# Optimization experiments

Hardware: AMD Instinct MI355X
Metric: run time of the kernel (lower is better)

Reference implementation:

```python
import jax, jax.numpy as jnp
from jax import lax
import numpy as np

DN = ('NCHW', 'OIHW', 'NCHW')

def conv(x, w, b, stride, pad):
    y = lax.conv_general_dilated(x, w, (stride, stride), [(pad, pad), (pad, pad)], dimension_numbers=DN)
    return y if b is None else y + b[None, :, None, None]

def conv_transpose(x, w, b):
    # torch ConvTranspose2d(k=4, s=2, p=1); w in torch layout (Cin, Cout, 4, 4)
    w_f = jnp.flip(w, (2, 3)).transpose(1, 0, 2, 3)  # -> OIHW, flipped
    y = lax.conv_general_dilated(x, w_f, (1, 1), [(2, 2), (2, 2)], lhs_dilation=(2, 2), dimension_numbers=DN)
    return y + b[None, :, None, None]

def res_stack(x, w3, w1, n_layers=2):
    # shared weights across layers (ModuleList([layer]*n) aliases one module)
    for _ in range(n_layers):
        h = conv(jax.nn.relu(x), w3, None, 1, 1)
        h = conv(jax.nn.relu(h), w1, None, 1, 0)
        x = x + h
    return jax.nn.relu(x)

def setup_inputs() -> dict:
    key = jax.random.key(0)
    ks = jax.random.split(key, 16)
    s = 0.02
    d = {
        'x': jax.random.normal(ks[0], (32, 3, 256, 256), jnp.float32),
        'enc_w1': jax.random.normal(ks[1], (128, 3, 4, 4), jnp.float32) * s,
        'enc_b1': jnp.zeros((128,), jnp.float32),
        'enc_w2': jax.random.normal(ks[2], (256, 128, 4, 4), jnp.float32) * s,
        'enc_b2': jnp.zeros((256,), jnp.float32),
        'enc_w3': jax.random.normal(ks[3], (512, 256, 4, 4), jnp.float32) * s,
        'enc_b3': jnp.zeros((512,), jnp.float32),
        'enc_res_w3': jax.random.normal(ks[4], (32, 512, 3, 3), jnp.float32) * s,
        'enc_res_w1': jax.random.normal(ks[5], (512, 32, 1, 1), jnp.float32) * s,
        'prevq_w': jax.random.normal(ks[6], (64, 512, 1, 1), jnp.float32) * s,
        'prevq_b': jnp.zeros((64,), jnp.float32),
        'emb': jax.random.normal(ks[7], (512, 64), jnp.float32),
        'dec_w1': jax.random.normal(ks[8], (64, 256, 4, 4), jnp.float32) * s,
        'dec_b1': jnp.zeros((256,), jnp.float32),
        'dec_res_w3': jax.random.normal(ks[9], (32, 256, 3, 3), jnp.float32) * s,
        'dec_res_w1': jax.random.normal(ks[10], (256, 32, 1, 1), jnp.float32) * s,
        'dec_w2': jax.random.normal(ks[11], (256, 128, 4, 4), jnp.float32) * s,
        'dec_b2': jnp.zeros((128,), jnp.float32),
        'dec_w3': jax.random.normal(ks[12], (128, 3, 4, 4), jnp.float32) * s,
        'dec_b3': jnp.zeros((3,), jnp.float32),
    }
    return d

def vqvae_fwd(x, enc_w1, enc_b1, enc_w2, enc_b2, enc_w3, enc_b3, enc_res_w3, enc_res_w1,
              prevq_w, prevq_b, emb, dec_w1, dec_b1, dec_res_w3, dec_res_w1,
              dec_w2, dec_b2, dec_w3, dec_b3):
    # encoder
    z = jax.nn.relu(conv(x, enc_w1, enc_b1, 2, 1))
    z = jax.nn.relu(conv(z, enc_w2, enc_b2, 2, 1))
    z = conv(z, enc_w3, enc_b3, 2, 1)
    z = res_stack(z, enc_res_w3, enc_res_w1)
    z_e = conv(z, prevq_w, prevq_b, 1, 0)  # (B, D=64, 32, 32)
    # vector quantiser
    B, C, H, W = z_e.shape
    x_flat = z_e.reshape(B, C, H * W).transpose(0, 2, 1)  # (B, HW, D)
    d2 = (jnp.sum(x_flat ** 2, -1, keepdims=True)
          - 2.0 * jnp.einsum('bnd,kd->bnk', x_flat, emb)
          + jnp.sum(emb ** 2, -1))
    idx = jnp.argmin(d2, axis=2)  # (B, HW)
    z_q_flat = emb[idx]  # (B, HW, D)
    z_q = z_q_flat.transpose(0, 2, 1).reshape(B, C, H, W)
    sg = lax.stop_gradient
    q_loss = jnp.mean((sg(z_q_flat) - x_flat) ** 2) + jnp.mean((z_q_flat - sg(x_flat)) ** 2)
    # decoder
    y = conv_transpose(z_q, dec_w1, dec_b1)  # (B, 256, 64, 64)
    y = res_stack(y, dec_res_w3, dec_res_w1)
    y = jax.nn.relu(conv_transpose(y, dec_w2, dec_b2))
    y = conv_transpose(y, dec_w3, dec_b3)  # (B, 3, 256, 256)
    return y, q_loss

def reference(x, enc_w1, enc_b1, enc_w2, enc_b2, enc_w3, enc_b3, enc_res_w3, enc_res_w1,
              prevq_w, prevq_b, emb, dec_w1, dec_b1, dec_res_w3, dec_res_w1,
              dec_w2, dec_b2, dec_w3, dec_b3):
    return vqvae_fwd(x, enc_w1, enc_b1, enc_w2, enc_b2, enc_w3, enc_b3, enc_res_w3, enc_res_w1,
                     prevq_w, prevq_b, emb, dec_w1, dec_b1, dec_res_w3, dec_res_w1,
                     dec_w2, dec_b2, dec_w3, dec_b3)
```

## Files before the change

kernel.cpp:

```cpp
#include <hip/hip_runtime.h>

typedef __attribute__((ext_vector_type(8))) short short8;
typedef __attribute__((ext_vector_type(4))) float f32x4;
typedef __attribute__((ext_vector_type(4))) unsigned int uint4v;

__device__ __forceinline__ unsigned short f2bf(float f) {
  unsigned u = __builtin_bit_cast(unsigned, f);
  u = (u + 0x7FFFu + ((u >> 16) & 1u)) >> 16;
  return (unsigned short)u;
}
__device__ __forceinline__ float bf2f(unsigned short h) {
  unsigned u = ((unsigned)h) << 16;
  return __builtin_bit_cast(float, u);
}

template<int TMT, int MODE, bool SPLIT, bool RELU_IN, bool RELU_OUT, bool BIAS, bool ACCUM>
__global__ __launch_bounds__(256) void k_mfconv(
    const float* __restrict__ in, const unsigned short* __restrict__ wp,
    const float* __restrict__ bias, float* __restrict__ out,
    int Ci, int inW, int inH, int pWSH, int pHWSH,
    int Co, int ntap, int ntt,
    unsigned syp, unsigned sxp,
    int outW, int outHW) {
  const int tid  = threadIdx.x;
  const int lane = tid & 63, wave = tid >> 6;
  const int pW  = 1 << pWSH;
  const int pHW = 1 << pHWSH;
  const int inHW = inW * inH;
  const int nk32 = Ci >> 5;
  const int KS   = (nk32 >= 2) ? 2 : 1;
  const int NITS = 4 * KS;
  const int cpt  = nk32 / KS;
  const int total = ntap * cpt;

  int bx = blockIdx.x;
  const int gx = gridDim.x;
  if ((gx & 7) == 0) bx = (bx & 7) * (gx >> 3) + (bx >> 3);
  const int n0  = bx * 64;
  const int coG = blockIdx.y;
  const int ph  = (MODE == 1) ? blockIdx.z : 0;
  const int tap0 = (MODE == 1) ? ph * 4 : 0;
  const int pdy = ph >> 1, pdx = ph & 1;

  constexpr int NPL = SPLIT ? 2 : 1;
  constexpr int PL = 64 * 70;
  __shared__ __align__(16) unsigned short Bs[2 * NPL * PL];

  const int px  = lane;
  const int p   = n0 + px;
  const int img = p >> pHWSH;
  const int rem = p & (pHW - 1);
  const int y   = rem >> pWSH;
  const int x   = rem & (pW - 1);
  const size_t base_img = (size_t)img * Ci * inHW;

  constexpr int NTO = (TMT == 4) ? 4 : 2;
  const int mt = (TMT == 4) ? wave : (wave & 1);
  const int ntb = (TMT == 4) ? 0 : ((wave >> 1) * 2);
  f32x4 acc[NTO];
#pragma unroll
  for (int u = 0; u < NTO; ++u) acc[u] = (f32x4){0.f, 0.f, 0.f, 0.f};

  const int cp = wave;
  float v[16];

  auto ldr = [&](int tap_, int chunk_) {
    const int T = tap0 + tap_;
    const int dy = (int)((syp >> (2 * T)) & 3u) - 1;
    const int dx = (int)((sxp >> (2 * T)) & 3u) - 1;
    const int ys = (MODE == 2) ? (2 * y + dy) : (y + dy);
    const int xs = (MODE == 2) ? (2 * x + dx) : (x + dx);
    const bool ok = ((unsigned)ys < (unsigned)inH) && ((unsigned)xs < (unsigned)inW);
    const float* __restrict__ ipb = in + base_img + (ptrdiff_t)ys * inW + xs;
    const int ci0 = chunk_ * (KS * 32);
#pragma unroll
    for (int it2 = 0; it2 < 8; ++it2) {
      if (it2 >= NITS) break;
      const int cl = 2 * (cp + 4 * it2);
      float a = 0.f, b = 0.f;
      if (ok) {
        a = ipb[(size_t)(ci0 + cl) * inHW];
        b = ipb[(size_t)(ci0 + cl + 1) * inHW];
      }
      if (RELU_IN) { a = fmaxf(a, 0.f); b = fmaxf(b, 0.f); }
      v[2 * it2] = a; v[2 * it2 + 1] = b;
    }
  };
  auto pwr = [&](int b) {
#pragma unroll
    for (int it2 = 0; it2 < 8; ++it2) {
      if (it2 >= NITS) break;
      const int cl = 2 * (cp + 4 * it2);
      float a = v[2 * it2], c = v[2 * it2 + 1];
      unsigned short h0 = f2bf(a), h1 = f2bf(c);
      *(unsigned*)&Bs[(b * NPL) * PL + px * 70 + cl] = (unsigned)h0 | ((unsigned)h1 << 16);
      if (SPLIT) {
        unsigned short l0 = f2bf(a - bf2f(h0)), l1 = f2bf(c - bf2f(h1));
        *(unsigned*)&Bs[(b * NPL + 1) * PL + px * 70 + cl] = (unsigned)l0 | ((unsigned)l1 << 16);
      }
    }
  };

  ldr(0, 0);
  pwr(0);
  __syncthreads();

  int tap = 0, chunk = 0;
  for (int it = 0; it < total; ++it) {
    const int b = it & 1;
    const int T = tap0 + tap;
    short8 ah[2], al[2];
#pragma unroll
    for (int s = 0; s < 2; ++s) {
      if (s >= KS) break;
      const int cic = chunk * KS + s;
      size_t abase;
      if (SPLIT) abase = ((((size_t)coG * ntt + T) * nk32 + cic) * 2 * TMT + mt) * 512;
      else       abase = ((((size_t)coG * ntt + T) * nk32 + cic) * TMT + mt) * 512;
      ah[s] = *(const short8*)(wp + abase + (size_t)lane * 8);
      if (SPLIT) al[s] = *(const short8*)(wp + abase + (size_t)TMT * 512 + (size_t)lane * 8);
    }
    int tap2 = tap, chunk2 = chunk + 1;
    if (chunk2 == cpt) { chunk2 = 0; tap2 = tap + 1; }
    const bool more = (it + 1 < total);
    if (more) ldr(tap2, chunk2);
#pragma unroll
    for (int s = 0; s < 2; ++s) {
      if (s >= KS) break;
#pragma unroll
      for (int u = 0; u < NTO; ++u) {
        const int row = 16 * (ntb + u) + (lane & 15);
        const unsigned* bp = (const unsigned*)&Bs[(b * NPL) * PL + row * 70 + s * 32 + (lane >> 4) * 8];
        uint4v hv = {bp[0], bp[1], bp[2], bp[3]};
        short8 bh = __builtin_bit_cast(short8, hv);
        acc[u] = __builtin_amdgcn_mfma_f32_16x16x32_bf16(ah[s], bh, acc[u], 0, 0, 0);
        if (SPLIT) {
          const unsigned* bpl = bp + (PL >> 1);
          uint4v lv = {bpl[0], bpl[1], bpl[2], bpl[3]};
          short8 bl = __builtin_bit_cast(short8, lv);
          acc[u] = __builtin_amdgcn_mfma_f32_16x16x32_bf16(al[s], bh, acc[u], 0, 0, 0);
          acc[u] = __builtin_amdgcn_mfma_f32_16x16x32_bf16(ah[s], bl, acc[u], 0, 0, 0);
        }
      }
    }
    if (more) {
      pwr(b ^ 1);
      __syncthreads();
    }
    tap = tap2; chunk = chunk2;
  }

#pragma unroll
  for (int u = 0; u < NTO; ++u) {
    const int nt = ntb + u;
    const int pn = n0 + nt * 16 + (lane & 15);
    const int img2 = pn >> pHWSH;
    const int rem2 = pn & (pHW - 1);
    const int y2 = rem2 >> pWSH, x2 = rem2 & (pW - 1);
    int oy, ox;
    if (MODE == 1) { oy = 2 * y2 + pdy; ox = 2 * x2 + pdx; }
    else           { oy = y2;           ox = x2; }
#pragma unroll
    for (int r = 0; r < 4; ++r) {
      const int co = coG * (TMT * 16) + mt * 16 + (lane >> 4) * 4 + r;
      float val = acc[u][r];
      if (BIAS) val += bias[co];
      if (RELU_OUT) val = fmaxf(val, 0.f);
      size_t oi = ((size_t)img2 * Co + co) * outHW + (size_t)oy * outW + ox;
      if (ACCUM) out[oi] += val; else out[oi] = val;
    }
  }
}

template<bool SPLIT>
__global__ __launch_bounds__(256) void k_pack_o(
    const float* __restrict__ w, unsigned short* __restrict__ p,
    int Co, int Ci, int ntap, int TMT, int E) {
  int i = blockIdx.x * 256 + threadIdx.x;
  if (i >= E) return;
  const int NC = Ci >> 5;
  int j = i & 7, lane = (i >> 3) & 63, r = i >> 9;
  int mt = r % TMT; r /= TMT;
  int sp = 0;
  if (SPLIT) { sp = r % 2; r /= 2; }
  int cic = r % NC; r /= NC;
  int T = r % ntap; int coG = r / ntap;
  int co = coG * (TMT * 16) + mt * 16 + (lane & 15);
  int ci = cic * 32 + (lane >> 4) * 8 + j;
  float wv = w[((size_t)co * Ci + ci) * ntap + T];
  unsigned short hv = f2bf(wv);
  p[i] = (SPLIT && sp == 1) ? f2bf(wv - bf2f(hv)) : hv;
}

__global__ __launch_bounds__(256) void k_pack_ct(
    const float* __restrict__ w, unsigned short* __restrict__ p,
    int Ci, int Co, int TMT, int E) {
  int i = blockIdx.x * 256 + threadIdx.x;
  if (i >= E) return;
  const int NC = Ci >> 5;
  int j = i & 7, lane = (i >> 3) & 63, r = i >> 9;
  int mt = r % TMT; r /= TMT;
  int cic = r % NC; r /= NC;
  int T = r % 16;   int coG = r / 16;
  int phx = T >> 2, t = T & 3;
  int dy = phx >> 1, dx = phx & 1, ty = t >> 1, tx = t & 1;
  int ky = 2 * ty + 1 - dy, kx = 2 * tx + 1 - dx;
  int co = coG * (TMT * 16) + mt * 16 + (lane & 15);
  int ci = cic * 32 + (lane >> 4) * 8 + j;
  p[i] = f2bf(w[(((size_t)ci * Co + co) * 4 + ky) * 4 + kx]);
}

template<int COB, bool RELU_OUT>
__global__ __launch_bounds__(256) void k_conv4(
    const float* __restrict__ in, const float* __restrict__ w,
    const float* __restrict__ bias, float* __restrict__ out,
    int N, int Ci, int Hi, int Wi, int Co) {
  const int Ho = Hi >> 1, Wo = Wi >> 1;
  const int ow = blockIdx.x * 16 + (threadIdx.x & 15);
  const int oh = blockIdx.y * 16 + (threadIdx.x >> 4);
  const int zcnt = Co / COB;
  const int co0 = (blockIdx.z % zcnt) * COB;
  const int n   = blockIdx.z / zcnt;
  if (oh >= Ho || ow >= Wo) return;
  const float* __restrict__ ip = in + (size_t)n * Ci * Hi * Wi;
  float acc[COB];
#pragma unroll
  for (int j = 0; j < COB; ++j) acc[j] = bias[co0 + j];
  const int ih0 = 2 * oh - 1, iw0 = 2 * ow - 1;
  for (int ci = 0; ci < Ci; ++ci) {
    const float* __restrict__ ic = ip + (size_t)ci * Hi * Wi;
    float v[16];
#pragma unroll
    for (int kh = 0; kh < 4; ++kh) {
      const int ih = ih0 + kh;
      const bool hok = (unsigned)ih < (unsigned)Hi;
      const float* __restrict__ irow = ic + (long)ih * Wi;
#pragma unroll
      for (int kw = 0; kw < 4; ++kw) {
        const int iw = iw0 + kw;
        v[kh * 4 + kw] = (hok && (unsigned)iw < (unsigned)Wi) ? irow[iw] : 0.f;
      }
    }
#pragma unroll
    for (int j = 0; j < COB; ++j) {
      const float* __restrict__ wc = w + ((size_t)(co0 + j) * Ci + ci) * 16;
#pragma unroll
      for (int t = 0; t < 16; ++t) acc[j] = fmaf(v[t], wc[t], acc[j]);
    }
  }
#pragma unroll
  for (int j = 0; j < COB; ++j) {
    float a = acc[j];
    if (RELU_OUT) a = fmaxf(a, 0.f);
    out[(((size_t)n * Co + co0 + j) * Ho + oh) * Wo + ow] = a;
  }
}

template<int COB, bool RELU_IN, int CSPLIT>
__global__ __launch_bounds__(256) void k_conv3(
    const float* __restrict__ in, const float* __restrict__ w,
    float* __restrict__ out, int N, int Ci, int H, int W, int Co) {
  const int ow = blockIdx.x * 16 + (threadIdx.x & 15);
  const int oh = blockIdx.y * 16 + (threadIdx.x >> 4);
  const int zcnt = Co / COB;
  const int z = blockIdx.z;
  const int cs  = z % CSPLIT;
  const int co0 = ((z / CSPLIT) % zcnt) * COB;
  const int n   = z / (CSPLIT * zcnt);
  if (oh >= H || ow >= W) return;
  const int CPS = Ci / CSPLIT;
  const float* __restrict__ ip = in + (size_t)n * Ci * H * W;
  float acc[COB];
#pragma unroll
  for (int j = 0; j < COB; ++j) acc[j] = 0.f;
  for (int ci = cs * CPS; ci < (cs + 1) * CPS; ++ci) {
    const float* __restrict__ ic = ip + (size_t)ci * H * W;
    float v[9];
#pragma unroll
    for (int kh = 0; kh < 3; ++kh) {
      const int ih = oh - 1 + kh;
      const bool hok = (unsigned)ih < (unsigned)H;
      const float* __restrict__ irow = ic + (long)ih * W;
#pragma unroll
      for (int kw = 0; kw < 3; ++kw) {
        const int iw = ow - 1 + kw;
        float t = (hok && (unsigned)iw < (unsigned)W) ? irow[iw] : 0.f;
        if (RELU_IN) t = fmaxf(t, 0.f);
        v[kh * 3 + kw] = t;
      }
    }
#pragma unroll
    for (int j = 0; j < COB; ++j) {
      const float* __restrict__ wc = w + ((size_t)(co0 + j) * Ci + ci) * 9;
#pragma unroll
      for (int t = 0; t < 9; ++t) acc[j] = fmaf(v[t], wc[t], acc[j]);
    }
  }
#pragma unroll
  for (int j = 0; j < COB; ++j) {
    size_t oi = (((size_t)n * Co + co0 + j) * H + oh) * W + ow;
    if (CSPLIT > 1) atomicAdd(&out[oi], acc[j]);
    else out[oi] = acc[j];
  }
}

template<int COB, bool RELU_IN, bool ACCUM>
__global__ __launch_bounds__(256) void k_conv1(
    const float* __restrict__ in, const float* __restrict__ w,
    const float* __restrict__ bias, float* __restrict__ out,
    int N, int Ci, int P, int Co) {
  const int p = blockIdx.x * 256 + threadIdx.x;
  const int co0 = blockIdx.y * COB;
  const int n = blockIdx.z;
  if (p >= P) return;
  float acc[COB];
#pragma unroll
  for (int j = 0; j < COB; ++j) acc[j] = bias ? bias[co0 + j] : 0.f;
  const float* __restrict__ ip = in + (size_t)n * Ci * P + p;
#pragma unroll 8
  for (int ci = 0; ci < Ci; ++ci) {
    float v = ip[(size_t)ci * P];
    if (RELU_IN) v = fmaxf(v, 0.f);
#pragma unroll
    for (int j = 0; j < COB; ++j)
      acc[j] = fmaf(v, w[(size_t)(co0 + j) * Ci + ci], acc[j]);
  }
#pragma unroll
  for (int j = 0; j < COB; ++j) {
    size_t oi = ((size_t)n * Co + co0 + j) * P + p;
    if (ACCUM) out[oi] += acc[j]; else out[oi] = acc[j];
  }
}

template<int COB, bool RELU_IN, bool RELU_OUT>
__global__ __launch_bounds__(256) void k_convT(
    const float* __restrict__ in, const float* __restrict__ w,
    const float* __restrict__ bias, float* __restrict__ out,
    int N, int Ci, int Hi, int Wi, int Co) {
  const int Ho = Hi * 2, Wo = Wi * 2;
  const int x = blockIdx.x * 16 + (threadIdx.x & 15);
  const int y = blockIdx.y * 16 + (threadIdx.x >> 4);
  const int zcnt = Co / COB;
  const int co0 = (blockIdx.z % zcnt) * COB;
  const int n   = blockIdx.z / zcnt;
  if (x >= Wi || y >= Hi) return;
  const float* __restrict__ ip = in + (size_t)n * Ci * Hi * Wi;
  float a00[COB], a01[COB], a10[COB], a11[COB];
#pragma unroll
  for (int j = 0; j < COB; ++j) {
    float b = bias[co0 + j];
    a00[j] = b; a01[j] = b; a10[j] = b; a11[j] = b;
  }
  const bool r0 = y > 0, r2 = y + 1 < Hi, c0 = x > 0, c2 = x + 1 < Wi;
#pragma unroll 2
  for (int ci = 0; ci < Ci; ++ci) {
    const float* __restrict__ ic = ip + (size_t)ci * Hi * Wi + (size_t)y * Wi + x;
    float v00 = 0.f, v01 = 0.f, v02 = 0.f, v10 = 0.f, v12 = 0.f,
          v20 = 0.f, v21 = 0.f, v22 = 0.f;
    float v11 = ic[0];
    if (c0) v10 = ic[-1];
    if (c2) v12 = ic[1];
    if (r0) { v01 = ic[-Wi]; if (c0) v00 = ic[-Wi - 1]; if (c2) v02 = ic[-Wi + 1]; }
    if (r2) { v21 = ic[Wi];  if (c0) v20 = ic[Wi - 1];  if (c2) v22 = ic[Wi + 1]; }
    if (RELU_IN) {
      v00 = fmaxf(v00, 0.f); v01 = fmaxf(v01, 0.f); v02 = fmaxf(v02, 0.f);
      v10 = fmaxf(v10, 0.f); v11 = fmaxf(v11, 0.f); v12 = fmaxf(v12, 0.f);
      v20 = fmaxf(v20, 0.f); v21 = fmaxf(v21, 0.f); v22 = fmaxf(v22, 0.f);
    }
#pragma unroll
    for (int j = 0; j < COB; ++j) {
      const float* __restrict__ wc = w + ((size_t)ci * Co + co0 + j) * 16;
      a00[j] = fmaf(v11, wc[5],  fmaf(v10, wc[7],  fmaf(v01, wc[13], fmaf(v00, wc[15], a00[j]))));
      a01[j] = fmaf(v12, wc[4],  fmaf(v11, wc[6],  fmaf(v02, wc[12], fmaf(v01, wc[14], a01[j]))));
      a10[j] = fmaf(v21, wc[1],  fmaf(v20, wc[3],  fmaf(v11, wc[9],  fmaf(v10, wc[11], a10[j]))));
      a11[j] = fmaf(v22, wc[0],  fmaf(v21, wc[2],  fmaf(v12, wc[8],  fmaf(v11, wc[10], a11[j]))));
    }
  }
#pragma unroll
  for (int j = 0; j < COB; ++j) {
    size_t b = ((size_t)n * Co + co0 + j) * Ho;
    float o00 = a00[j], o01 = a01[j], o10 = a10[j], o11 = a11[j];
    if (RELU_OUT) {
      o00 = fmaxf(o00, 0.f); o01 = fmaxf(o01, 0.f);
      o10 = fmaxf(o10, 0.f); o11 = fmaxf(o11, 0.f);
    }
    out[(b + 2 * y) * Wo + 2 * x]         = o00;
    out[(b + 2 * y) * Wo + 2 * x + 1]     = o01;
    out[(b + 2 * y + 1) * Wo + 2 * x]     = o10;
    out[(b + 2 * y + 1) * Wo + 2 * x + 1] = o11;
  }
}

__global__ __launch_bounds__(256, 2) void k_vq(
    const float* __restrict__ ze, const float* __restrict__ emb,
    float* __restrict__ zq, float* __restrict__ loss) {
  __shared__ float e2s[512];
  const int tid = threadIdx.x;
  for (int k = tid; k < 512; k += 256) {
    const f32x4* e4 = (const f32x4*)(emb + (size_t)k * 64);
    float s = 0.f;
#pragma unroll
    for (int dq = 0; dq < 16; ++dq) {
      f32x4 ev = e4[dq];
      s = fmaf(ev[0], ev[0], s); s = fmaf(ev[1], ev[1], s);
      s = fmaf(ev[2], ev[2], s); s = fmaf(ev[3], ev[3], s);
    }
    e2s[k] = s;
  }
  __syncthreads();
  const int p = blockIdx.x * 256 + tid;
  const int n = p >> 10, px = p & 1023;
  float xv[64];
  const float* __restrict__ zp = ze + (size_t)n * 64 * 1024 + px;
#pragma unroll
  for (int d = 0; d < 64; ++d) xv[d] = zp[(size_t)d * 1024];
  float best = 1e30f; int bi = 0;
  for (int k = 0; k < 512; ++k) {
    const f32x4* e4 = (const f32x4*)(emb + (size_t)k * 64);
    float dot = 0.f;
#pragma unroll
    for (int dq = 0; dq < 16; ++dq) {
      f32x4 ev = e4[dq];
      dot = fmaf(xv[4 * dq],     ev[0], dot);
      dot = fmaf(xv[4 * dq + 1], ev[1], dot);
      dot = fmaf(xv[4 * dq + 2], ev[2], dot);
      dot = fmaf(xv[4 * dq + 3], ev[3], dot);
    }
    float sc = fmaf(-2.f, dot, e2s[k]);
    if (sc < best) { best = sc; bi = k; }
  }
  const float* __restrict__ eb = emb + (size_t)bi * 64;
  float* __restrict__ qp = zq + (size_t)n * 64 * 1024 + px;
  float l = 0.f;
#pragma unroll
  for (int d = 0; d < 64; ++d) {
    float ev = eb[d];
    qp[(size_t)d * 1024] = ev;
    float df = ev - xv[d];
    l = fmaf(df, df, l);
  }
#pragma unroll
  for (int off = 32; off > 0; off >>= 1) l += __shfl_down(l, off, 64);
  if ((tid & 63) == 0) atomicAdd(loss, l * (2.f / 2097152.f));
}

__global__ __launch_bounds__(64) void k_vq64(
    const float* __restrict__ ze, const float* __restrict__ emb,
    float* __restrict__ zq, float* __restrict__ loss,
    int N, int P, int K) {
  const int t = blockIdx.x * 64 + threadIdx.x;
  if (t >= N * P) return;
  const int n = t / P, p = t % P;
  float xv[64];
  const float* __restrict__ zp = ze + (size_t)n * 64 * P + p;
#pragma unroll
  for (int d = 0; d < 64; ++d) xv[d] = zp[(size_t)d * P];
  float best = 1e30f; int bi = 0;
  for (int k = 0; k < K; ++k) {
    const float* __restrict__ e = emb + (size_t)k * 64;
    float dot = 0.f, e2 = 0.f;
#pragma unroll
    for (int d = 0; d < 64; ++d) {
      float ev = e[d];
      dot = fmaf(xv[d], ev, dot);
      e2  = fmaf(ev, ev, e2);
    }
    float score = e2 - 2.f * dot;
    if (score < best) { best = score; bi = k; }
  }
  const float* __restrict__ eb = emb + (size_t)bi * 64;
  float* __restrict__ qp = zq + (size_t)n * 64 * P + p;
  float l = 0.f;
#pragma unroll
  for (int d = 0; d < 64; ++d) {
    float ev = eb[d];
    qp[(size_t)d * P] = ev;
    float df = ev - xv[d];
    l = fmaf(df, df, l);
  }
#pragma unroll
  for (int off = 32; off > 0; off >>= 1) l += __shfl_down(l, off, 64);
  if ((threadIdx.x & 63) == 0) atomicAdd(loss, l * (2.f / 2097152.f));
}

extern "C" void kernel_launch(void* const* d_in, const int* in_sizes, int n_in,
                              void* d_out, int out_size, void* d_ws, size_t ws_size,
                              hipStream_t stream) {
  const float* x    = (const float*)d_in[0];
  const float* ew1  = (const float*)d_in[1];
  const float* eb1  = (const float*)d_in[2];
  const float* ew2  = (const float*)d_in[3];
  const float* eb2  = (const float*)d_in[4];
  const float* ew3  = (const float*)d_in[5];
  const float* eb3  = (const float*)d_in[6];
  const float* erw3 = (const float*)d_in[7];
  const float* erw1 = (const float*)d_in[8];
  const float* pqw  = (const float*)d_in[9];
  const float* pqb  = (const float*)d_in[10];
  const float* emb  = (const float*)d_in[11];
  const float* dw1  = (const float*)d_in[12];
  const float* db1  = (const float*)d_in[13];
  const float* drw3 = (const float*)d_in[14];
  const float* drw1 = (const float*)d_in[15];
  const float* dw2  = (const float*)d_in[16];
  const float* db2  = (const float*)d_in[17];
  const float* dw3  = (const float*)d_in[18];
  const float* db3  = (const float*)d_in[19];
  float* out = (float*)d_out;
  char*  ws  = (char*)d_ws;
  float* loss = out + 6291456;
  const size_t MiB = 1048576ull, KiB = 1024ull;

  dim3 blk(256);
  hipMemsetAsync(loss, 0, 4, stream);

  unsigned syct = 0, sxct = 0;
  for (int T = 0; T < 16; ++T) {
    int phx = T >> 2, dy = phx >> 1, dx = phx & 1, t = T & 3, ty = t >> 1, tx = t & 1;
    int sy = (dy == 0) ? (ty ? -1 : 0) : (ty ? 0 : 1);
    int sx = (dx == 0) ? (tx ? -1 : 0) : (tx ? 0 : 1);
    syct |= (unsigned)(sy + 1) << (2 * T);
    sxct |= (unsigned)(sx + 1) << (2 * T);
  }
  unsigned syc3 = 0, sxc3 = 0;
  for (int t = 0; t < 9; ++t) {
    syc3 |= (unsigned)(t / 3) << (2 * t);
    sxc3 |= (unsigned)(t % 3) << (2 * t);
  }
  unsigned syc4 = 0, sxc4 = 0;
  for (int t = 0; t < 16; ++t) {
    syc4 |= (unsigned)(t / 4) << (2 * t);
    sxc4 |= (unsigned)(t % 4) << (2 * t);
  }
  const unsigned sy1 = 1, sx1 = 1;

  auto packs = [&](char* PB) {
    unsigned short* e2p   = (unsigned short*)(PB);
    unsigned short* e3p   = (unsigned short*)(PB + 2048 * KiB);
    unsigned short* erc3p = (unsigned short*)(PB + 10240 * KiB);
    unsigned short* erc1p = (unsigned short*)(PB + 10816 * KiB);
    unsigned short* pqp   = (unsigned short*)(PB + 10880 * KiB);
    unsigned short* d1p   = (unsigned short*)(PB + 11008 * KiB);
    unsigned short* d2p   = (unsigned short*)(PB + 11520 * KiB);
    unsigned short* dc3p  = (unsigned short*)(PB + 12544 * KiB);
    unsigned short* dc1p  = (unsigned short*)(PB + 12688 * KiB);
    k_pack_o<true ><<<dim3(1048576 / 256), blk, 0, stream>>>(ew2,  e2p,  256, 128, 16, 4, 1048576);
    k_pack_o<true ><<<dim3(4194304 / 256), blk, 0, stream>>>(ew3,  e3p,  512, 256, 16, 4, 4194304);
    k_pack_o<true ><<<dim3(294912 / 256),  blk, 0, stream>>>(erw3, erc3p, 32, 512,  9, 2, 294912);
    k_pack_o<true ><<<dim3(32768 / 256),   blk, 0, stream>>>(erw1, erc1p, 512, 32,  1, 4, 32768);
    k_pack_o<true ><<<dim3(65536 / 256),   blk, 0, stream>>>(pqw,  pqp,   64, 512,  1, 4, 65536);
    k_pack_ct<<<dim3(262144 / 256), blk, 0, stream>>>(dw1, d1p, 64, 256, 4, 262144);
    k_pack_ct<<<dim3(524288 / 256), blk, 0, stream>>>(dw2, d2p, 256, 128, 4, 524288);
    k_pack_o<false><<<dim3(73728 / 256),   blk, 0, stream>>>(drw3, dc3p,  32, 256,  9, 2, 73728);
    k_pack_o<false><<<dim3(8192 / 256),    blk, 0, stream>>>(drw1, dc1p, 256, 32,  1, 4, 8192);
  };

  if (ws_size >= 498ull * MiB) {
    float* z1 = (float*)ws;
    float* z2 = (float*)(ws + 256 * MiB);
    float* z3 = (float*)(ws + 384 * MiB);
    float* h  = (float*)(ws + 448 * MiB);
    float* ze = (float*)(ws + 452 * MiB);
    float* zq = (float*)(ws + 460 * MiB);
    float* hd = (float*)(ws + 468 * MiB);
    char*  PB = ws + 484 * MiB;
    unsigned short* e2p   = (unsigned short*)(PB);
    unsigned short* e3p   = (unsigned short*)(PB + 2048 * KiB);
    unsigned short* erc3p = (unsigned short*)(PB + 10240 * KiB);
    unsigned short* erc1p = (unsigned short*)(PB + 10816 * KiB);
    unsigned short* pqp   = (unsigned short*)(PB + 10880 * KiB);
    unsigned short* d1p   = (unsigned short*)(PB + 11008 * KiB);
    unsigned short* d2p   = (unsigned short*)(PB + 11520 * KiB);
    unsigned short* dc3p  = (unsigned short*)(PB + 12544 * KiB);
    unsigned short* dc1p  = (unsigned short*)(PB + 12688 * KiB);
    packs(PB);

    k_conv4<8, true><<<dim3(8, 8, 32 * 16), blk, 0, stream>>>(x, ew1, eb1, z1, 32, 3, 256, 256, 128);
    k_mfconv<4, 2, true, false, true, true, false><<<dim3(2048, 4), blk, 0, stream>>>(
        z1, e2p, eb2, z2, 128, 128, 128, 6, 12, 256, 16, 16, syc4, sxc4, 64, 4096);
    k_mfconv<4, 2, true, false, false, true, false><<<dim3(512, 8), blk, 0, stream>>>(
        z2, e3p, eb3, z3, 256, 64, 64, 5, 10, 512, 16, 16, syc4, sxc4, 32, 1024);
    for (int i = 0; i < 2; ++i) {
      k_mfconv<2, 0, true, true, false, false, false><<<dim3(512, 1), blk, 0, stream>>>(
          z3, erc3p, nullptr, h, 512, 32, 32, 5, 10, 32, 9, 9, syc3, sxc3, 32, 1024);
      k_mfconv<4, 0, true, true, false, false, true><<<dim3(512, 8), blk, 0, stream>>>(
          h, erc1p, nullptr, z3, 32, 32, 32, 5, 10, 512, 1, 1, sy1, sx1, 32, 1024);
    }
    k_mfconv<4, 0, true, true, false, true, false><<<dim3(512, 1), blk, 0, stream>>>(
        z3, pqp, pqb, ze, 512, 32, 32, 5, 10, 64, 1, 1, sy1, sx1, 32, 1024);
    k_vq<<<dim3(128), blk, 0, stream>>>(ze, emb, zq, loss);
    float* y1 = (float*)(ws + 256 * MiB);
    float* y2 = (float*)ws;
    k_mfconv<4, 1, false, false, false, true, false><<<dim3(512, 4, 4), blk, 0, stream>>>(
        zq, d1p, db1, y1, 64, 32, 32, 5, 10, 256, 4, 16, syct, sxct, 64, 4096);
    for (int i = 0; i < 2; ++i) {
      k_mfconv<2, 0, false, true, false, false, false><<<dim3(2048, 1), blk, 0, stream>>>(
          y1, dc3p, nullptr, hd, 256, 64, 64, 6, 12, 32, 9, 9, syc3, sxc3, 64, 4096);
      k_mfconv<4, 0, false, true, false, false, true><<<dim3(2048, 4), blk, 0, stream>>>(
          hd, dc1p, nullptr, y1, 32, 64, 64, 6, 12, 256, 1, 1, sy1, sx1, 64, 4096);
    }
    k_mfconv<4, 1, false, true, true, true, false><<<dim3(2048, 2, 4), blk, 0, stream>>>(
        y1, d2p, db2, y2, 256, 64, 64, 6, 12, 128, 4, 16, syct, sxct, 128, 16384);
    k_convT<3, false, false><<<dim3(8, 8, 32), blk, 0, stream>>>(y2, dw3, db3, out, 32, 128, 128, 128, 3);
    return;
  }

  if (ws_size >= 128ull * MiB) {
    float* z3  = (float*)ws;
    float* h   = (float*)(ws + 64 * MiB);
    float* ze  = (float*)(ws + 68 * MiB);
    float* zq  = (float*)(ws + 100 * MiB);
    char*  PB  = ws + 115 * MiB;
    unsigned short* e2p   = (unsigned short*)(PB);
    unsigned short* e3p   = (unsigned short*)(PB + 2048 * KiB);
    unsigned short* erc3p = (unsigned short*)(PB + 10240 * KiB);
    unsigned short* erc1p = (unsigned short*)(PB + 10816 * KiB);
    unsigned short* pqp   = (unsigned short*)(PB + 10880 * KiB);
    unsigned short* d1p   = (unsigned short*)(PB + 11008 * KiB);
    unsigned short* d2p   = (unsigned short*)(PB + 11520 * KiB);
    unsigned short* dc3p  = (unsigned short*)(PB + 12544 * KiB);
    unsigned short* dc1p  = (unsigned short*)(PB + 12688 * KiB);
    packs(PB);

    const int NE = 4;
    float* z1c = (float*)(ws + 64 * MiB);
    float* z2c = (float*)(ws + 96 * MiB);
    for (int n0 = 0; n0 < 32; n0 += NE) {
      const float* xb = x + (size_t)n0 * 3 * 65536;
      float* z3b = z3 + (size_t)n0 * 512 * 1024;
      k_conv4<8, true><<<dim3(8, 8, NE * 16), blk, 0, stream>>>(xb, ew1, eb1, z1c, NE, 3, 256, 256, 128);
      k_mfconv<4, 2, true, false, true, true, false><<<dim3(256, 4), blk, 0, stream>>>(
          z1c, e2p, eb2, z2c, 128, 128, 128, 6, 12, 256, 16, 16, syc4, sxc4, 64, 4096);
      k_mfconv<4, 2, true, false, false, true, false><<<dim3(64, 8), blk, 0, stream>>>(
          z2c, e3p, eb3, z3b, 256, 64, 64, 5, 10, 512, 16, 16, syc4, sxc4, 32, 1024);
    }
    for (int i = 0; i < 2; ++i) {
      k_mfconv<2, 0, true, true, false, false, false><<<dim3(512, 1), blk, 0, stream>>>(
          z3, erc3p, nullptr, h, 512, 32, 32, 5, 10, 32, 9, 9, syc3, sxc3, 32, 1024);
      k_mfconv<4, 0, true, true, false, false, true><<<dim3(512, 8), blk, 0, stream>>>(
          h, erc1p, nullptr, z3, 32, 32, 32, 5, 10, 512, 1, 1, sy1, sx1, 32, 1024);
    }
    k_mfconv<4, 0, true, true, false, true, false><<<dim3(512, 1), blk, 0, stream>>>(
        z3, pqp, pqb, ze, 512, 32, 32, 5, 10, 64, 1, 1, sy1, sx1, 32, 1024);
    k_vq<<<dim3(128), blk, 0, stream>>>(ze, emb, zq, loss);

    const int ND = 8;
    float* y1c = (float*)ws;
    float* hd  = (float*)(ws + 32 * MiB);
    float* y2c = (float*)(ws + 36 * MiB);
    for (int c = 0; c < 32; c += ND) {
      const float* zqb = zq + (size_t)c * 64 * 1024;
      float* outb = out + (size_t)c * 3 * 65536;
      k_mfconv<4, 1, false, false, false, true, false><<<dim3(128, 4, 4), blk, 0, stream>>>(
          zqb, d1p, db1, y1c, 64, 32, 32, 5, 10, 256, 4, 16, syct, sxct, 64, 4096);
      for (int i = 0; i < 2; ++i) {
        k_mfconv<2, 0, false, true, false, false, false><<<dim3(512, 1), blk, 0, stream>>>(
            y1c, dc3p, nullptr, hd, 256, 64, 64, 6, 12, 32, 9, 9, syc3, sxc3, 64, 4096);
        k_mfconv<4, 0, false, true, false, false, true><<<dim3(512, 4), blk, 0, stream>>>(
            hd, dc1p, nullptr, y1c, 32, 64, 64, 6, 12, 256, 1, 1, sy1, sx1, 64, 4096);
      }
      k_mfconv<4, 1, false, true, true, true, false><<<dim3(512, 2, 4), blk, 0, stream>>>(
          y1c, d2p, db2, y2c, 256, 64, 64, 6, 12, 128, 4, 16, syct, sxct, 128, 16384);
      k_convT<3, false, false><<<dim3(8, 8, ND), blk, 0, stream>>>(y2c, dw3, db3, outb, ND, 128, 128, 128, 3);
    }
    return;
  }

  const size_t PER_IMG = 12582912ull;
  int NB = (int)(ws_size / PER_IMG);
  if (NB > 32) NB = 32;
  if (NB < 1)  NB = 1;

  for (int n0 = 0; n0 < 32; n0 += NB) {
    const int nb = (32 - n0 < NB) ? (32 - n0) : NB;
    const float* xb   = x   + (size_t)n0 * 3 * 65536;
    float*       outb = out + (size_t)n0 * 3 * 65536;

    float* z1 = (float*)ws;
    float* z2 = (float*)(ws + (size_t)NB * 8388608ull);
    float* z3 = (float*)ws;
    char*  tb = ws + (size_t)NB * 2097152ull;
    float* he = (float*)tb;
    float* ze = (float*)(tb + (size_t)NB * 131072ull);
    float* zq = (float*)(tb + (size_t)NB * 393216ull);
    float* hd = (float*)(tb + (size_t)NB * 655360ull);
    float* y1 = z2;
    float* y2 = (float*)ws;

    k_conv4<4, true ><<<dim3(8, 8, nb * 32), blk, 0, stream>>>(xb, ew1, eb1, z1, nb,   3, 256, 256, 128);
    k_conv4<4, true ><<<dim3(4, 4, nb * 64), blk, 0, stream>>>(z1, ew2, eb2, z2, nb, 128, 128, 128, 256);
    k_conv4<4, false><<<dim3(2, 2, nb * 128), blk, 0, stream>>>(z2, ew3, eb3, z3, nb, 256,  64,  64, 512);
    for (int i = 0; i < 2; ++i) {
      k_conv3<4, true, 1><<<dim3(2, 2, nb * 8), blk, 0, stream>>>(z3, erw3, he, nb, 512, 32, 32, 32);
      k_conv1<8, true, true><<<dim3(4, 64, nb), blk, 0, stream>>>(he, erw1, nullptr, z3, nb, 32, 1024, 512);
    }
    k_conv1<8, true, false><<<dim3(4, 8, nb), blk, 0, stream>>>(z3, pqw, pqb, ze, nb, 512, 1024, 64);
    k_vq64<<<dim3(nb * 16), dim3(64), 0, stream>>>(ze, emb, zq, loss, nb, 1024, 512);
    k_convT<4, false, false><<<dim3(2, 2, nb * 64), blk, 0, stream>>>(zq, dw1, db1, y1, nb,  64, 32, 32, 256);
    for (int i = 0; i < 2; ++i) {
      k_conv3<4, true, 1><<<dim3(4, 4, nb * 8), blk, 0, stream>>>(y1, drw3, hd, nb, 256, 64, 64, 32);
      k_conv1<8, true, true><<<dim3(16, 32, nb), blk, 0, stream>>>(hd, drw1, nullptr, y1, nb, 32, 4096, 256);
    }
    k_convT<4, true, true ><<<dim3(4, 4, nb * 32), blk, 0, stream>>>(y1, dw2, db2, y2, nb, 256, 64, 64, 128);
    k_convT<1, false, false><<<dim3(8, 8, nb * 3), blk, 0, stream>>>(y2, dw3, db3, outb, nb, 128, 128, 128, 3);
  }
}
```

Before: 4.899 ms.

## Widen MFMA conv tiles to 128 output channels and move first encoder conv to MFMA

Adds an MT template parameter so each wave computes two 16-row output-channel tiles, reusing the staged activation tile across twice as many channels. Grids shrink by half in the channel dimension and weights are repacked with a TMT of 8. It also replaces the scalar first encoder conv with an MFMA implicit-GEMM kernel, padding 3 input channels to 4 and using bf16 hi/lo split. Packing moves to the hip bf16 intrinsic, and launch bounds now request 4 blocks per SIMD, which raises register pressure from the doubled accumulators.

```diff
diff --git a/kernel.cpp b/kernel.cpp
--- a/kernel.cpp
+++ b/kernel.cpp
@@ -1,4 +1,5 @@
 #include <hip/hip_runtime.h>
+#include <hip/hip_bf16.h>
 
 typedef __attribute__((ext_vector_type(8))) short short8;
 typedef __attribute__((ext_vector_type(4))) float f32x4;
@@ -13,9 +14,15 @@
   unsigned u = ((unsigned)h) << 16;
   return __builtin_bit_cast(float, u);
 }
-
-template<int TMT, int MODE, bool SPLIT, bool RELU_IN, bool RELU_OUT, bool BIAS, bool ACCUM>
-__global__ __launch_bounds__(256) void k_mfconv(
+__device__ __forceinline__ unsigned pk_bf16(float a, float b) {
+  __hip_bfloat162 h = __float22bfloat162_rn(make_float2(a, b));
+  unsigned u;
+  __builtin_memcpy(&u, &h, 4);
+  return u;
+}
+
+template<int TMT, int MT, int MODE, bool SPLIT, bool RELU_IN, bool RELU_OUT, bool BIAS, bool ACCUM>
+__global__ __launch_bounds__(256, 4) void k_mfconv(
     const float* __restrict__ in, const unsigned short* __restrict__ wp,
     const float* __restrict__ bias, float* __restrict__ out,
     int Ci, int inW, int inH, int pWSH, int pHWSH,
@@ -32,6 +39,7 @@
   const int NITS = 4 * KS;
   const int cpt  = nk32 / KS;
   const int total = ntap * cpt;
+  constexpr int TT = TMT * MT;
 
   int bx = blockIdx.x;
   const int gx = gridDim.x;
@@ -55,11 +63,11 @@
   const size_t base_img = (size_t)img * Ci * inHW;
 
   constexpr int NTO = (TMT == 4) ? 4 : 2;
-  const int mt = (TMT == 4) ? wave : (wave & 1);
+  const int mt0 = (TMT == 4) ? wave : (wave & 1);
   const int ntb = (TMT == 4) ? 0 : ((wave >> 1) * 2);
-  f32x4 acc[NTO];
-#pragma unroll
-  for (int u = 0; u < NTO; ++u) acc[u] = (f32x4){0.f, 0.f, 0.f, 0.f};
+  f32x4 acc[MT * NTO];
+#pragma unroll
+  for (int u = 0; u < MT * NTO; ++u) acc[u] = (f32x4){0.f, 0.f, 0.f, 0.f};
 
   const int cp = wave;
   float v[16];
@@ -92,11 +100,11 @@
       if (it2 >= NITS) break;
       const int cl = 2 * (cp + 4 * it2);
       float a = v[2 * it2], c = v[2 * it2 + 1];
-      unsigned short h0 = f2bf(a), h1 = f2bf(c);
-      *(unsigned*)&Bs[(b * NPL) * PL + px * 70 + cl] = (unsigned)h0 | ((unsigned)h1 << 16);
+      unsigned hp = pk_bf16(a, c);
+      *(unsigned*)&Bs[(b * NPL) * PL + px * 70 + cl] = hp;
       if (SPLIT) {
-        unsigned short l0 = f2bf(a - bf2f(h0)), l1 = f2bf(c - bf2f(h1));
-        *(unsigned*)&Bs[(b * NPL + 1) * PL + px * 70 + cl] = (unsigned)l0 | ((unsigned)l1 << 16);
+        float h0 = bf2f((unsigned short)hp), h1 = bf2f((unsigned short)(hp >> 16));
+        *(unsigned*)&Bs[(b * NPL + 1) * PL + px * 70 + cl] = pk_bf16(a - h0, c - h1);
       }
     }
   };
@@ -109,17 +117,6 @@
   for (int it = 0; it < total; ++it) {
     const int b = it & 1;
     const int T = tap0 + tap;
-    short8 ah[2], al[2];
-#pragma unroll
-    for (int s = 0; s < 2; ++s) {
-      if (s >= KS) break;
-      const int cic = chunk * KS + s;
-      size_t abase;
-      if (SPLIT) abase = ((((size_t)coG * ntt + T) * nk32 + cic) * 2 * TMT + mt) * 512;
-      else       abase = ((((size_t)coG * ntt + T) * nk32 + cic) * TMT + mt) * 512;
-      ah[s] = *(const short8*)(wp + abase + (size_t)lane * 8);
-      if (SPLIT) al[s] = *(const short8*)(wp + abase + (size_t)TMT * 512 + (size_t)lane * 8);
-    }
     int tap2 = tap, chunk2 = chunk + 1;
     if (chunk2 == cpt) { chunk2 = 0; tap2 = tap + 1; }
     const bool more = (it + 1 < total);
@@ -127,21 +124,42 @@
 #pragma unroll
     for (int s = 0; s < 2; ++s) {
       if (s >= KS) break;
+      const int cic = chunk * KS + s;
+      short8 ah[MT], al[MT];
+#pragma unroll
+      for (int m = 0; m < MT; ++m) {
+        const int mtm = mt0 + m * TMT;
+        size_t abase;
+        if (SPLIT) abase = ((((size_t)coG * ntt + T) * nk32 + cic) * 2 * TT + mtm) * 512;
+        else       abase = ((((size_t)coG * ntt + T) * nk32 + cic) * TT + mtm) * 512;
+        ah[m] = *(const short8*)(wp + abase + (size_t)lane * 8);
+        if (SPLIT) al[m] = *(const short8*)(wp + abase + (size_t)TT * 512 + (size_t)lane * 8);
+      }
+      short8 bh[NTO], bl[NTO];
 #pragma unroll
       for (int u = 0; u < NTO; ++u) {
         const int row = 16 * (ntb + u) + (lane & 15);
         const unsigned* bp = (const unsigned*)&Bs[(b * NPL) * PL + row * 70 + s * 32 + (lane >> 4) * 8];
         uint4v hv = {bp[0], bp[1], bp[2], bp[3]};
-        short8 bh = __builtin_bit_cast(short8, hv);
-        acc[u] = __builtin_amdgcn_mfma_f32_16x16x32_bf16(ah[s], bh, acc[u], 0, 0, 0);
+        bh[u] = __builtin_bit_cast(short8, hv);
         if (SPLIT) {
           const unsigned* bpl = bp + (PL >> 1);
           uint4v lv = {bpl[0], bpl[1], bpl[2], bpl[3]};
-          short8 bl = __builtin_bit_cast(short8, lv);
-          acc[u] = __builtin_amdgcn_mfma_f32_16x16x32_bf16(al[s], bh, acc[u], 0, 0, 0);
-          acc[u] = __builtin_amdgcn_mfma_f32_16x16x32_bf16(ah[s], bl, acc[u], 0, 0, 0);
+          bl[u] = __builtin_bit_cast(short8, lv);
         }
       }
+#pragma unroll
+      for (int m = 0; m < MT; ++m)
+#pragma unroll
+        for (int u = 0; u < NTO; ++u) {
+          f32x4 a = acc[m * NTO + u];
+          a = __builtin_amdgcn_mfma_f32_16x16x32_bf16(ah[m], bh[u], a, 0, 0, 0);
+          if (SPLIT) {
+            a = __builtin_amdgcn_mfma_f32_16x16x32_bf16(al[m], bh[u], a, 0, 0, 0);
+            a = __builtin_amdgcn_mfma_f32_16x16x32_bf16(ah[m], bl[u], a, 0, 0, 0);
+          }
+          acc[m * NTO + u] = a;
+        }
     }
     if (more) {
       pwr(b ^ 1);
@@ -151,25 +169,113 @@
   }
 
 #pragma unroll
-  for (int u = 0; u < NTO; ++u) {
-    const int nt = ntb + u;
-    const int pn = n0 + nt * 16 + (lane & 15);
-    const int img2 = pn >> pHWSH;
-    const int rem2 = pn & (pHW - 1);
-    const int y2 = rem2 >> pWSH, x2 = rem2 & (pW - 1);
-    int oy, ox;
-    if (MODE == 1) { oy = 2 * y2 + pdy; ox = 2 * x2 + pdx; }
-    else           { oy = y2;           ox = x2; }
-#pragma unroll
-    for (int r = 0; r < 4; ++r) {
-      const int co = coG * (TMT * 16) + mt * 16 + (lane >> 4) * 4 + r;
-      float val = acc[u][r];
-      if (BIAS) val += bias[co];
-      if (RELU_OUT) val = fmaxf(val, 0.f);
-      size_t oi = ((size_t)img2 * Co + co) * outHW + (size_t)oy * outW + ox;
-      if (ACCUM) out[oi] += val; else out[oi] = val;
-    }
-  }
+  for (int m = 0; m < MT; ++m) {
+    const int mtm = mt0 + m * TMT;
+#pragma unroll
+    for (int u = 0; u < NTO; ++u) {
+      const int nt = ntb + u;
+      const int pn = n0 + nt * 16 + (lane & 15);
+      const int img2 = pn >> pHWSH;
+      const int rem2 = pn & (pHW - 1);
+      const int y2 = rem2 >> pWSH, x2 = rem2 & (pW - 1);
+      int oy, ox;
+      if (MODE == 1) { oy = 2 * y2 + pdy; ox = 2 * x2 + pdx; }
+      else           { oy = y2;           ox = x2; }
+#pragma unroll
+      for (int r = 0; r < 4; ++r) {
+        const int co = coG * (TT * 16) + mtm * 16 + (lane >> 4) * 4 + r;
+        float val = acc[m * NTO + u][r];
+        if (BIAS) val += bias[co];
+        if (RELU_OUT) val = fmaxf(val, 0.f);
+        size_t oi = ((size_t)img2 * Co + co) * outHW + (size_t)oy * outW + ox;
+        if (ACCUM) out[oi] += val; else out[oi] = val;
+      }
+    }
+  }
+}
+
+__global__ __launch_bounds__(256, 4) void k_mfenc1(
+    const float* __restrict__ in, const unsigned short* __restrict__ wp,
+    const float* __restrict__ bias, float* __restrict__ out) {
+  const int tid = threadIdx.x, lane = tid & 63, wave = tid >> 6;
+  int bx = blockIdx.x;
+  const int gx = gridDim.x;
+  if ((gx & 7) == 0) bx = (bx & 7) * (gx >> 3) + (bx >> 3);
+  const int n0 = bx * 64;
+  const int p = n0 + lane;
+  const int img = p >> 14;
+  const int rem = p & 16383;
+  const int y = rem >> 7, x = rem & 127;
+  __shared__ __align__(16) unsigned short Bs[2 * 4480];
+  const float* __restrict__ ib = in + (size_t)img * 3 * 65536;
+#pragma unroll
+  for (int i = 0; i < 8; ++i) {
+    const int kk0 = 2 * (wave + 4 * i);
+    float vv[2];
+#pragma unroll
+    for (int q = 0; q < 2; ++q) {
+      const int kk = kk0 + q;
+      const int tap = kk >> 2, c = kk & 3;
+      const int iy = 2 * y + (tap >> 2) - 1, ix = 2 * x + (tap & 3) - 1;
+      const bool ok = (c < 3) && ((unsigned)iy < 256u) && ((unsigned)ix < 256u);
+      vv[q] = ok ? ib[((size_t)c << 16) + (size_t)iy * 256 + ix] : 0.f;
+    }
+    unsigned hp = pk_bf16(vv[0], vv[1]);
+    *(unsigned*)&Bs[lane * 70 + kk0] = hp;
+    float h0 = bf2f((unsigned short)hp), h1 = bf2f((unsigned short)(hp >> 16));
+    *(unsigned*)&Bs[4480 + lane * 70 + kk0] = pk_bf16(vv[0] - h0, vv[1] - h1);
+  }
+  __syncthreads();
+
+  f32x4 acc[8];
+#pragma unroll
+  for (int u = 0; u < 8; ++u) acc[u] = (f32x4){0.f, 0.f, 0.f, 0.f};
+#pragma unroll
+  for (int s = 0; s < 2; ++s) {
+    short8 ah[2], al[2];
+#pragma unroll
+    for (int m = 0; m < 2; ++m) {
+      const int mtm = wave + m * 4;
+      size_t abase = (((size_t)s * 2 + 0) * 8 + mtm) * 512;
+      ah[m] = *(const short8*)(wp + abase + (size_t)lane * 8);
+      al[m] = *(const short8*)(wp + abase + 8 * 512 + (size_t)lane * 8);
+    }
+    short8 bh[4], bl[4];
+#pragma unroll
+    for (int u = 0; u < 4; ++u) {
+      const int row = 16 * u + (lane & 15);
+      const unsigned* bp = (const unsigned*)&Bs[row * 70 + s * 32 + (lane >> 4) * 8];
+      uint4v hv = {bp[0], bp[1], bp[2], bp[3]};
+      bh[u] = __builtin_bit_cast(short8, hv);
+      const unsigned* bpl = bp + 2240;
+      uint4v lv = {bpl[0], bpl[1], bpl[2], bpl[3]};
+      bl[u] = __builtin_bit_cast(short8, lv);
+    }
+#pragma unroll
+    for (int m = 0; m < 2; ++m)
+#pragma unroll
+      for (int u = 0; u < 4; ++u) {
+        f32x4 a = acc[m * 4 + u];
+        a = __builtin_amdgcn_mfma_f32_16x16x32_bf16(ah[m], bh[u], a, 0, 0, 0);
+        a = __builtin_amdgcn_mfma_f32_16x16x32_bf16(al[m], bh[u], a, 0, 0, 0);
+        a = __builtin_amdgcn_mfma_f32_16x16x32_bf16(ah[m], bl[u], a, 0, 0, 0);
+        acc[m * 4 + u] = a;
+      }
+  }
+#pragma unroll
+  for (int m = 0; m < 2; ++m)
+#pragma unroll
+    for (int u = 0; u < 4; ++u) {
+      const int pn = n0 + u * 16 + (lane & 15);
+      const int img2 = pn >> 14;
+      const int rem2 = pn & 16383;
+#pragma unroll
+      for (int r = 0; r < 4; ++r) {
+        const int co = (wave + m * 4) * 16 + (lane >> 4) * 4 + r;
+        float val = fmaxf(acc[m * 4 + u][r] + bias[co], 0.f);
+        out[((size_t)img2 * 128 + co) * 16384 + rem2] = val;
+      }
+    }
 }
 
 template<bool SPLIT>
@@ -208,6 +314,21 @@
   int co = coG * (TMT * 16) + mt * 16 + (lane & 15);
   int ci = cic * 32 + (lane >> 4) * 8 + j;
   p[i] = f2bf(w[(((size_t)ci * Co + co) * 4 + ky) * 4 + kx]);
+}
+
+__global__ __launch_bounds__(256) void k_pack_e1(
+    const float* __restrict__ w, unsigned short* __restrict__ p) {
+  int i = blockIdx.x * 256 + threadIdx.x;
+  int j = i & 7, lane = (i >> 3) & 63, r = i >> 9;
+  int mt = r % 8; r /= 8;
+  int sp = r % 2; r /= 2;
+  int cic = r;
+  int co = mt * 16 + (lane & 15);
+  int kk = cic * 32 + (lane >> 4) * 8 + j;
+  int tap = kk >> 2, c = kk & 3;
+  float wv = (c < 3) ? w[(((size_t)co * 3 + c) * 4 + (tap >> 2)) * 4 + (tap & 3)] : 0.f;
+  unsigned short hv = f2bf(wv);
+  p[i] = (sp == 1) ? f2bf(wv - bf2f(hv)) : hv;
 }
 
 template<int COB, bool RELU_OUT>
@@ -544,15 +665,17 @@
     unsigned short* d2p   = (unsigned short*)(PB + 11520 * KiB);
     unsigned short* dc3p  = (unsigned short*)(PB + 12544 * KiB);
     unsigned short* dc1p  = (unsigned short*)(PB + 12688 * KiB);
-    k_pack_o<true ><<<dim3(1048576 / 256), blk, 0, stream>>>(ew2,  e2p,  256, 128, 16, 4, 1048576);
-    k_pack_o<true ><<<dim3(4194304 / 256), blk, 0, stream>>>(ew3,  e3p,  512, 256, 16, 4, 4194304);
+    unsigned short* e1p   = (unsigned short*)(PB + 12704 * KiB);
+    k_pack_o<true ><<<dim3(1048576 / 256), blk, 0, stream>>>(ew2,  e2p,  256, 128, 16, 8, 1048576);
+    k_pack_o<true ><<<dim3(4194304 / 256), blk, 0, stream>>>(ew3,  e3p,  512, 256, 16, 8, 4194304);
     k_pack_o<true ><<<dim3(294912 / 256),  blk, 0, stream>>>(erw3, erc3p, 32, 512,  9, 2, 294912);
-    k_pack_o<true ><<<dim3(32768 / 256),   blk, 0, stream>>>(erw1, erc1p, 512, 32,  1, 4, 32768);
+    k_pack_o<true ><<<dim3(32768 / 256),   blk, 0, stream>>>(erw1, erc1p, 512, 32,  1, 8, 32768);
     k_pack_o<true ><<<dim3(65536 / 256),   blk, 0, stream>>>(pqw,  pqp,   64, 512,  1, 4, 65536);
-    k_pack_ct<<<dim3(262144 / 256), blk, 0, stream>>>(dw1, d1p, 64, 256, 4, 262144);
-    k_pack_ct<<<dim3(524288 / 256), blk, 0, stream>>>(dw2, d2p, 256, 128, 4, 524288);
+    k_pack_ct<<<dim3(262144 / 256), blk, 0, stream>>>(dw1, d1p, 64, 256, 8, 262144);
+    k_pack_ct<<<dim3(524288 / 256), blk, 0, stream>>>(dw2, d2p, 256, 128, 8, 524288);
     k_pack_o<false><<<dim3(73728 / 256),   blk, 0, stream>>>(drw3, dc3p,  32, 256,  9, 2, 73728);
-    k_pack_o<false><<<dim3(8192 / 256),    blk, 0, stream>>>(drw1, dc1p, 256, 32,  1, 4, 8192);
+    k_pack_o<false><<<dim3(8192 / 256),    blk, 0, stream>>>(drw1, dc1p, 256, 32,  1, 8, 8192);
+    k_pack_e1<<<dim3(256), blk, 0, stream>>>(ew1, e1p);
   };
 
   if (ws_size >= 498ull * MiB) {
@@ -573,33 +696,34 @@
     unsigned short* d2p   = (unsigned short*)(PB + 11520 * KiB);
     unsigned short* dc3p  = (unsigned short*)(PB + 12544 * KiB);
     unsigned short* dc1p  = (unsigned short*)(PB + 12688 * KiB);
+    unsigned short* e1p   = (unsigned short*)(PB + 12704 * KiB);
     packs(PB);
 
-    k_conv4<8, true><<<dim3(8, 8, 32 * 16), blk, 0, stream>>>(x, ew1, eb1, z1, 32, 3, 256, 256, 128);
-    k_mfconv<4, 2, true, false, true, true, false><<<dim3(2048, 4), blk, 0, stream>>>(
+    k_mfenc1<<<dim3(8192), blk, 0, stream>>>(x, e1p, eb1, z1);
+    k_mfconv<4, 2, 2, true, false, true, true, false><<<dim3(2048, 2), blk, 0, stream>>>(
         z1, e2p, eb2, z2, 128, 128, 128, 6, 12, 256, 16, 16, syc4, sxc4, 64, 4096);
-    k_mfconv<4, 2, true, false, false, true, false><<<dim3(512, 8), blk, 0, stream>>>(
+    k_mfconv<4, 2, 2, true, false, false, true, false><<<dim3(512, 4), blk, 0, stream>>>(
         z2, e3p, eb3, z3, 256, 64, 64, 5, 10, 512, 16, 16, syc4, sxc4, 32, 1024);
     for (int i = 0; i < 2; ++i) {
-      k_mfconv<2, 0, true, true, false, false, false><<<dim3(512, 1), blk, 0, stream>>>(
+      k_mfconv<2, 1, 0, true, true, false, false, false><<<dim3(512, 1), blk, 0, stream>>>(
           z3, erc3p, nullptr, h, 512, 32, 32, 5, 10, 32, 9, 9, syc3, sxc3, 32, 1024);
-      k_mfconv<4, 0, true, true, false, false, true><<<dim3(512, 8), blk, 0, stream>>>(
+      k_mfconv<4, 2, 0, true, true, false, false, true><<<dim3(512, 4), blk, 0, stream>>>(
           h, erc1p, nullptr, z3, 32, 32, 32, 5, 10, 512, 1, 1, sy1, sx1, 32, 1024);
     }
-    k_mfconv<4, 0, true, true, false, true, false><<<dim3(512, 1), blk, 0, stream>>>(
+    k_mfconv<4, 1, 0, true, true, false, true, false><<<dim3(512, 1), blk, 0, stream>>>(
         z3, pqp, pqb, ze, 512, 32, 32, 5, 10, 64, 1, 1, sy1, sx1, 32, 1024);
     k_vq<<<dim3(128), blk, 0, stream>>>(ze, emb, zq, loss);
     float* y1 = (float*)(ws + 256 * MiB);
     float* y2 = (float*)ws;
-    k_mfconv<4, 1, false, false, false, true, false><<<dim3(512, 4, 4), blk, 0, stream>>>(
+    k_mfconv<4, 2, 1, false, false, false, true, false><<<dim3(512, 2, 4), blk, 0, stream>>>(
         zq, d1p, db1, y1, 64, 32, 32, 5, 10, 256, 4, 16, syct, sxct, 64, 4096);
     for (int i = 0; i < 2; ++i) {
-      k_mfconv<2, 0, false, true, false, false, false><<<dim3(2048, 1), blk, 0, stream>>>(
+      k_mfconv<2, 1, 0, false, true, false, false, false><<<dim3(2048, 1), blk, 0, stream>>>(
           y1, dc3p, nullptr, hd, 256, 64, 64, 6, 12, 32, 9, 9, syc3, sxc3, 64, 4096);
-      k_mfconv<4, 0, false, true, false, false, true><<<dim3(2048, 4), blk, 0, stream>>>(
+      k_mfconv<4, 2, 0, false, true, false, false, true><<<dim3(2048, 2), blk, 0, stream>>>(
           hd, dc1p, nullptr, y1, 32, 64, 64, 6, 12, 256, 1, 1, sy1, sx1, 64, 4096);
     }
-    k_mfconv<4, 1, false, true, true, true, false><<<dim3(2048, 2, 4), blk, 0, stream>>>(
+    k_mfconv<4, 2, 1, false, true, true, true, false><<<dim3(2048, 1, 4), blk, 0, stream>>>(
         y1, d2p, db2, y2, 256, 64, 64, 6, 12, 128, 4, 16, syct, sxct, 128, 16384);
     k_convT<3, false, false><<<dim3(8, 8, 32), blk, 0, stream>>>(y2, dw3, db3, out, 32, 128, 128, 128, 3);
     return;
@@ -620,6 +744,7 @@
     unsigned short* d2p   = (unsigned short*)(PB + 11520 * KiB);
     unsigned short* dc3p  = (unsigned short*)(PB + 12544 * KiB);
     unsigned short* dc1p  = (unsigned short*)(PB + 12688 * KiB);
+    unsigned short* e1p   = (unsigned short*)(PB + 12704 * KiB);
     packs(PB);
 
     const int NE = 4;
@@ -628,19 +753,19 @@
     for (int n0 = 0; n0 < 32; n0 += NE) {
       const float* xb = x + (size_t)n0 * 3 * 65536;
       float* z3b = z3 + (size_t)n0 * 512 * 1024;
-      k_conv4<8, true><<<dim3(8, 8, NE * 16), blk, 0, stream>>>(xb, ew1, eb1, z1c, NE, 3, 256, 256, 128);
-      k_mfconv<4, 2, true, false, true, true, false><<<dim3(256, 4), blk, 0, stream>>>(
+      k_mfenc1<<<dim3(NE * 256), blk, 0, stream>>>(xb, e1p, eb1, z1c);
+      k_mfconv<4, 2, 2, true, false, true, true, false><<<dim3(256, 2), blk, 0, stream>>>(
           z1c, e2p, eb2, z2c, 128, 128, 128, 6, 12, 256, 16, 16, syc4, sxc4, 64, 4096);
-      k_mfconv<4, 2, true, false, false, true, false><<<dim3(64, 8), blk, 0, stream>>>(
+      k_mfconv<4, 2, 2, true, false, false, true, false><<<dim3(64, 4), blk, 0, stream>>>(
           z2c, e3p, eb3, z3b, 256, 64, 64, 5, 10, 512, 16, 16, syc4, sxc4, 32, 1024);
     }
     for (int i = 0; i < 2; ++i) {
-      k_mfconv<2, 0, true, true, false, false, false><<<dim3(512, 1), blk, 0, stream>>>(
+      k_mfconv<2, 1, 0, true, true, false, false, false><<<dim3(512, 1), blk, 0, stream>>>(
           z3, erc3p, nullptr, h, 512, 32, 32, 5, 10, 32, 9, 9, syc3, sxc3, 32, 1024);
-      k_mfconv<4, 0, true, true, false, false, true><<<dim3(512, 8), blk, 0, stream>>>(
+      k_mfconv<4, 2, 0, true, true, false, false, true><<<dim3(512, 4), blk, 0, stream>>>(
           h, erc1p, nullptr, z3, 32, 32, 32, 5, 10, 512, 1, 1, sy1, sx1, 32, 1024);
     }
-    k_mfconv<4, 0, true, true, false, true, false><<<dim3(512, 1), blk, 0, stream>>>(
+    k_mfconv<4, 1, 0, true, true, false, true, false><<<dim3(512, 1), blk, 0, stream>>>(
         z3, pqp, pqb, ze, 512, 32, 32, 5, 10, 64, 1, 1, sy1, sx1, 32, 1024);
     k_vq<<<dim3(128), blk, 0, stream>>>(ze, emb, zq, loss);
 
@@ -651,15 +776,15 @@
     for (int c = 0; c < 32; c += ND) {
       const float* zqb = zq + (size_t)c * 64 * 1024;
       float* outb = out + (size_t)c * 3 * 65536;
-      k_mfconv<4, 1, false, false, false, true, false><<<dim3(128, 4, 4), blk, 0, stream>>>(
+      k_mfconv<4, 2, 1, false, false, false, true, false><<<dim3(128, 2, 4), blk, 0, stream>>>(
           zqb, d1p, db1, y1c, 64, 32, 32, 5, 10, 256, 4, 16, syct, sxct, 64, 4096);
       for (int i = 0; i < 2; ++i) {
-        k_mfconv<2, 0, false, true, false, false, false><<<dim3(512, 1), blk, 0, stream>>>(
+        k_mfconv<2, 1, 0, false, true, false, false, false><<<dim3(512, 1), blk, 0, stream>>>(
             y1c, dc3p, nullptr, hd, 256, 64, 64, 6, 12, 32, 9, 9, syc3, sxc3, 64, 4096);
-        k_mfconv<4, 0, false, true, false, false, true><<<dim3(512, 4), blk, 0, stream>>>(
+        k_mfconv<4, 2, 0, false, true, false, false, true><<<dim3(512, 2), blk, 0, stream>>>(
             hd, dc1p, nullptr, y1c, 32, 64, 64, 6, 12, 256, 1, 1, sy1, sx1, 64, 4096);
       }
-      k_mfconv<4, 1, false, true, true, true, false><<<dim3(512, 2, 4), blk, 0, stream>>>(
+      k_mfconv<4, 2, 1, false, true, true, true, false><<<dim3(512, 1, 4), blk, 0, stream>>>(
           y1c, d2p, db2, y2c, 256, 64, 64, 6, 12, 128, 4, 16, syct, sxct, 128, 16384);
       k_convT<3, false, false><<<dim3(8, 8, ND), blk, 0, stream>>>(y2c, dw3, db3, outb, ND, 128, 128, 128, 3);
     }
```

After: 4.290 ms. -12.4%, faster.
